# Kernel tuning notes

Hardware: AMD Instinct MI355X
Metric: run time of the kernel (lower is better)

The kernel has to match this reference:

```python
import jax, jax.numpy as jnp
import numpy as np

B = 131072
N_STEPS = 216
H = 1.0 / 216.0            # Euler step size
A_Z0 = 0.005               # baseline wander amplitude (mV)
F2 = 0.25                  # baseline wander frequency (Hz)
OMEGA = 2.0 * np.pi        # angular velocity (rrpc = 1 s RR interval)
X0 = -0.417750770388669
Y0 = -0.9085616622823985
MIN_VAL = -0.01563
MAX_VAL = 0.042557


def setup_inputs() -> dict:
    key = jax.random.key(0)
    k1, k2 = jax.random.split(key)
    x = jax.random.uniform(k1, (B, 15), dtype=jnp.float32)   # [a,b,theta] x 5 waves, interleaved
    v0 = jax.random.normal(k2, (B,), dtype=jnp.float32) * 0.01
    return {"x": x, "v0": v0}


def _euler_integrate(params, v0):
    # params: [B,15] interleaved (a_i, b_i, theta_i) for P,Q,R,S,T waves
    a = params[:, 0::3]      # [B,5]
    b = params[:, 1::3]      # [B,5]
    theta = params[:, 2::3]  # [B,5]
    bsz = params.shape[0]
    dt = params.dtype
    x0 = jnp.full((bsz,), X0, dtype=dt)
    y0 = jnp.full((bsz,), Y0, dtype=dt)

    def step(carry, t):
        x, y, z = carry
        alpha = 1.0 - jnp.sqrt(x * x + y * y)
        f_x = alpha * x - OMEGA * y
        f_y = alpha * y + OMEGA * x
        th = jnp.arctan2(y, x)                      # [B]
        dth = jnp.fmod(th[:, None] - theta, 2.0 * np.pi)  # [B,5]
        gauss = a * dth * jnp.exp(-(dth * dth) / (2.0 * b * b))
        z0_t = A_Z0 * jnp.sin(2.0 * np.pi * F2 * t)
        f_z = -jnp.sum(gauss, axis=1) - (z - z0_t)
        x_n = x + H * f_x
        y_n = y + H * f_y
        z_n = z + H * f_z
        return (x_n, y_n, z_n), z_n

    ts = jnp.arange(N_STEPS, dtype=dt) / 216.0      # t=0 for step 0, then +1/216 each step
    _, z_t = jax.lax.scan(step, (x0, y0, v0.astype(dt)), ts)
    return z_t.T                                    # [B,216]


def _scale_signal(z):
    zmin = jnp.min(z, axis=1, keepdims=True)
    zmax = jnp.max(z, axis=1, keepdims=True)
    return (z - zmin) * MAX_VAL / (zmax - zmin) + MIN_VAL


def reference(x, v0):
    z = _euler_integrate(x, v0)
    return _scale_signal(z)
```

## Files before the change

kernel.cpp:

```cpp
#include <hip/hip_runtime.h>
#include <math.h>

#define NSTEPS 216
#define BLK 64
#define ZSTRIDE 217

__device__ float g_th[NSTEPS];
__device__ float g_z0[NSTEPS];

__global__ void traj_kernel() {
    const int t = threadIdx.x;
    if (t < NSTEPS) {
        float tf = (float)t / 216.0f;
        g_z0[t] = 0.005f * sinf((float)(0.5 * M_PI) * tf);
    }
    if (t == 0) {
        float x = (float)(-0.417750770388669);
        float y = (float)(-0.9085616622823985);
        const float W = (float)(2.0 * M_PI);
        const float H = (float)(1.0 / 216.0);
        for (int n = 0; n < NSTEPS; ++n) {
            g_th[n] = atan2f(y, x);
            float alpha = 1.0f - sqrtf(x * x + y * y);
            float fx = alpha * x - W * y;
            float fy = alpha * y + W * x;
            x = x + H * fx;
            y = y + H * fy;
        }
    }
}

__global__ __launch_bounds__(BLK) void euler_kernel(const float* __restrict__ prm,
                                                    const float* __restrict__ v0,
                                                    float* __restrict__ out) {
    __shared__ float th_s[NSTEPS];
    __shared__ float z0_s[NSTEPS];
    __shared__ float sc_s[BLK];
    __shared__ float of_s[BLK];
    __shared__ _Float16 z_s[BLK * ZSTRIDE];

    const int tid = threadIdx.x;
    for (int i = tid; i < NSTEPS; i += BLK) {
        th_s[i] = g_th[i];
        z0_s[i] = g_z0[i];
    }

    const int b = blockIdx.x * BLK + tid;
    const float* p = prm + (size_t)b * 15;

    float aj[5], tj[5], cj[5];
#pragma unroll
    for (int j = 0; j < 5; ++j) {
        aj[j] = p[3 * j + 0];
        float bb = p[3 * j + 1];
        cj[j] = -1.0f / (2.0f * bb * bb);
        tj[j] = p[3 * j + 2];
    }

    float z = v0[b];
    float zmin = 3.4e38f, zmax = -3.4e38f;
    const float H = (float)(1.0 / 216.0);

    __syncthreads();

    _Float16* zrow = z_s + tid * ZSTRIDE;
#pragma unroll 4
    for (int t = 0; t < NSTEPS; ++t) {
        float th = th_s[t];
        float G = 0.0f;
#pragma unroll
        for (int j = 0; j < 5; ++j) {
            float d = th - tj[j];
            G += aj[j] * d * __expf(d * d * cj[j]);
        }
        float fz = z0_s[t] - z - G;
        z = z + H * fz;
        zmin = fminf(zmin, z);
        zmax = fmaxf(zmax, z);
        zrow[t] = (_Float16)z;
    }

    float s = 0.042557f / (zmax - zmin);
    sc_s[tid] = s;
    of_s[tid] = fmaf(-zmin, s, -0.01563f);

    __syncthreads();

    float* outB = out + (size_t)blockIdx.x * (BLK * NSTEPS);
    const int TOT = BLK * NSTEPS;
    for (int base = tid * 4; base < TOT; base += BLK * 4) {
        float4 v;
        float* vp = &v.x;
#pragma unroll
        for (int k = 0; k < 4; ++k) {
            int idx = base + k;
            int r = (int)(((unsigned long long)idx * 19884108ull) >> 32);
            int t = idx - r * 216;
            float zz = (float)z_s[r * ZSTRIDE + t];
            vp[k] = fmaf(zz, sc_s[r], of_s[r]);
        }
        *(float4*)(outB + base) = v;
    }
}

extern "C" void kernel_launch(void* const* d_in, const int* in_sizes, int n_in,
                              void* d_out, int out_size, void* d_ws, size_t ws_size,
                              hipStream_t stream) {
    const float* x  = (const float*)d_in[0];
    const float* v0 = (const float*)d_in[1];
    float* out = (float*)d_out;
    const int nb = in_sizes[1];

    hipLaunchKernelGGL(traj_kernel, dim3(1), dim3(256), 0, stream);
    hipLaunchKernelGGL(euler_kernel, dim3(nb / BLK), dim3(BLK), 0, stream, x, v0, out);
}
```

Baseline: 220.8 us.

## Recompute trajectory in second pass instead of storing fp16 history in LDS

Replaces the fp16 per-thread z history in shared memory with a two-pass scheme. The first pass finds min/max, and the second pass recomputes z and writes scaled outputs through a small chunked LDS staging buffer for coalesced stores. It also folds log(a) into the exp argument, premultiplies the baseline-wander term by H, and parallelizes atan2 in traj_kernel. The recompute doubles the exp-heavy arithmetic, but it cuts LDS use enough to raise occupancy and removes the fp16 rounding. log(a) is not finite for a=0 or negative a.

```diff
diff --git a/kernel.cpp b/kernel.cpp
--- a/kernel.cpp
+++ b/kernel.cpp
@@ -3,24 +3,23 @@
 
 #define NSTEPS 216
 #define BLK 64
-#define ZSTRIDE 217
+#define CT 54
+#define CSTR 55
 
 __device__ float g_th[NSTEPS];
-__device__ float g_z0[NSTEPS];
+__device__ float g_hz0[NSTEPS];
 
 __global__ void traj_kernel() {
+    __shared__ float xs[NSTEPS], ys[NSTEPS];
     const int t = threadIdx.x;
-    if (t < NSTEPS) {
-        float tf = (float)t / 216.0f;
-        g_z0[t] = 0.005f * sinf((float)(0.5 * M_PI) * tf);
-    }
     if (t == 0) {
         float x = (float)(-0.417750770388669);
         float y = (float)(-0.9085616622823985);
         const float W = (float)(2.0 * M_PI);
         const float H = (float)(1.0 / 216.0);
         for (int n = 0; n < NSTEPS; ++n) {
-            g_th[n] = atan2f(y, x);
+            xs[n] = x;
+            ys[n] = y;
             float alpha = 1.0f - sqrtf(x * x + y * y);
             float fx = alpha * x - W * y;
             float fy = alpha * y + W * x;
@@ -28,42 +27,48 @@
             y = y + H * fy;
         }
     }
+    __syncthreads();
+    if (t < NSTEPS) {
+        g_th[t] = atan2f(ys[t], xs[t]);
+        float tf = (float)t / 216.0f;
+        g_hz0[t] = (float)(1.0 / 216.0) * (0.005f * sinf(1.5707964f * tf));
+    }
 }
 
 __global__ __launch_bounds__(BLK) void euler_kernel(const float* __restrict__ prm,
                                                     const float* __restrict__ v0,
                                                     float* __restrict__ out) {
     __shared__ float th_s[NSTEPS];
-    __shared__ float z0_s[NSTEPS];
-    __shared__ float sc_s[BLK];
-    __shared__ float of_s[BLK];
-    __shared__ _Float16 z_s[BLK * ZSTRIDE];
+    __shared__ float hz0_s[NSTEPS];
+    __shared__ float st_s[BLK * CSTR];
 
     const int tid = threadIdx.x;
     for (int i = tid; i < NSTEPS; i += BLK) {
         th_s[i] = g_th[i];
-        z0_s[i] = g_z0[i];
+        hz0_s[i] = g_hz0[i];
     }
 
     const int b = blockIdx.x * BLK + tid;
     const float* p = prm + (size_t)b * 15;
 
-    float aj[5], tj[5], cj[5];
+    float tj[5], cj[5], la[5];
 #pragma unroll
     for (int j = 0; j < 5; ++j) {
-        aj[j] = p[3 * j + 0];
+        float a  = p[3 * j + 0];
         float bb = p[3 * j + 1];
+        tj[j] = p[3 * j + 2];
         cj[j] = -1.0f / (2.0f * bb * bb);
-        tj[j] = p[3 * j + 2];
+        la[j] = __logf(a);
     }
 
-    float z = v0[b];
-    float zmin = 3.4e38f, zmax = -3.4e38f;
+    const float zinit = v0[b];
     const float H = (float)(1.0 / 216.0);
+    const float K = 1.0f - H;
 
     __syncthreads();
 
-    _Float16* zrow = z_s + tid * ZSTRIDE;
+    float z = zinit;
+    float zmin = 3.4e38f, zmax = -3.4e38f;
 #pragma unroll 4
     for (int t = 0; t < NSTEPS; ++t) {
         float th = th_s[t];
@@ -71,35 +76,40 @@
 #pragma unroll
         for (int j = 0; j < 5; ++j) {
             float d = th - tj[j];
-            G += aj[j] * d * __expf(d * d * cj[j]);
+            G = fmaf(d, __expf(fmaf(d * d, cj[j], la[j])), G);
         }
-        float fz = z0_s[t] - z - G;
-        z = z + H * fz;
+        z = fmaf(z, K, fmaf(-H, G, hz0_s[t]));
         zmin = fminf(zmin, z);
         zmax = fmaxf(zmax, z);
-        zrow[t] = (_Float16)z;
     }
+    const float s = 0.042557f / (zmax - zmin);
+    const float o = fmaf(-zmin, s, -0.01563f);
 
-    float s = 0.042557f / (zmax - zmin);
-    sc_s[tid] = s;
-    of_s[tid] = fmaf(-zmin, s, -0.01563f);
-
-    __syncthreads();
-
+    z = zinit;
     float* outB = out + (size_t)blockIdx.x * (BLK * NSTEPS);
-    const int TOT = BLK * NSTEPS;
-    for (int base = tid * 4; base < TOT; base += BLK * 4) {
-        float4 v;
-        float* vp = &v.x;
+    for (int c0 = 0; c0 < NSTEPS; c0 += CT) {
+#pragma unroll 4
+        for (int tc = 0; tc < CT; ++tc) {
+            int t = c0 + tc;
+            float th = th_s[t];
+            float G = 0.0f;
 #pragma unroll
-        for (int k = 0; k < 4; ++k) {
-            int idx = base + k;
-            int r = (int)(((unsigned long long)idx * 19884108ull) >> 32);
-            int t = idx - r * 216;
-            float zz = (float)z_s[r * ZSTRIDE + t];
-            vp[k] = fmaf(zz, sc_s[r], of_s[r]);
+            for (int j = 0; j < 5; ++j) {
+                float d = th - tj[j];
+                G = fmaf(d, __expf(fmaf(d * d, cj[j], la[j])), G);
+            }
+            z = fmaf(z, K, fmaf(-H, G, hz0_s[t]));
+            st_s[tid * CSTR + tc] = fmaf(z, s, o);
         }
-        *(float4*)(outB + base) = v;
+        __syncthreads();
+#pragma unroll 6
+        for (int k = 0; k < CT; ++k) {
+            unsigned idx = (unsigned)tid + BLK * k;
+            unsigned r = idx / 54u;
+            unsigned tt = idx - r * 54u;
+            outB[r * NSTEPS + c0 + tt] = st_s[r * CSTR + tt];
+        }
+        __syncthreads();
     }
 }
 
```

Result: faster. 191.7 us (-13.2%).
